# Kernel optimization log

Hardware: AMD Instinct MI355X
Metric: run time of the kernel (lower is better)

## Reference

```python
import jax, jax.numpy as jnp
import numpy as np

# Static graph layout: B equal-size graphs of N nodes; first S nodes of each
# graph are 'sentence' nodes, the remaining N-S are 'other' nodes.
B, N, S, C = 64, 4096, 512, 128
TOTAL = B * N
E = 4_194_304          # avg degree 16
K_SENT = 3             # num_output_sentences
RATIO = 0.5
K_OTHER = int(np.ceil(RATIO * (N - S)))  # 1792 -> 1795 kept nodes per graph


def setup_inputs() -> dict:
    key = jax.random.key(0)
    k1, k2, k3 = jax.random.split(key, 3)
    x = jax.random.normal(k1, (TOTAL, C), dtype=jnp.float32)
    weight = jax.random.uniform(k2, (C,), dtype=jnp.float32)  # torch.rand(1, C)
    edge_index = jax.random.randint(k3, (2, E), 0, TOTAL, dtype=jnp.int32)
    batch = jnp.repeat(jnp.arange(B, dtype=jnp.int32), N)     # per-node graph id
    return {"x": x, "weight": weight, "edge_index": edge_index, "batch": batch}


def _pool(x, weight, edge_index, batch):
    # score_i = tanh(<x_i, w> / ||w||)   (min_score is None branch)
    score = jnp.tanh((x @ weight) / jnp.linalg.norm(weight))        # [TOTAL]
    score_b = score.reshape(B, N)

    # ragged-as-dense per-graph top-k (torch does dense reshape + sort + gather)
    base = (jnp.arange(B, dtype=jnp.int32) * N)[:, None]            # [B,1]
    _, sent_idx = jax.lax.top_k(score_b[:, :S], K_SENT)             # [B,K_SENT]
    _, other_idx = jax.lax.top_k(score_b[:, S:], K_OTHER)           # [B,K_OTHER]
    perm = jnp.concatenate([
        (sent_idx.astype(jnp.int32) + base).reshape(-1),            # all sentence picks first
        (other_idx.astype(jnp.int32) + S + base).reshape(-1),
    ])                                                              # [B*(K_SENT+K_OTHER)]

    x_out = x[perm] * score[perm][:, None]                          # multiplier == 1
    batch_out = batch[perm]

    # filter_adj: remap kept nodes to new ids; drop edges touching dropped nodes.
    node_map = jnp.full((TOTAL,), -1, dtype=jnp.int32).at[perm].set(
        jnp.arange(perm.shape[0], dtype=jnp.int32))
    row = node_map[edge_index[0]]
    col = node_map[edge_index[1]]
    keep = (row >= 0) & (col >= 0)
    # jit-friendly compaction: stable-sort kept edges to the front, pad tail with -1
    order = jnp.argsort(jnp.where(keep, 0, 1), stable=True)
    edge_index_new = jnp.stack([jnp.where(keep, row, -1)[order],
                                jnp.where(keep, col, -1)[order]])
    num_edges = keep.sum()
    return x_out, edge_index_new, batch_out, perm, score[perm], num_edges


def reference(x, weight, edge_index, batch):
    return _pool(x, weight, edge_index, batch)
```

## Files before the change

### kernel.cpp

```cpp
#include <hip/hip_runtime.h>
#include <hip/hip_bf16.h>
#include <stdint.h>

#define NB 64
#define NN 4096
#define NS 512
#define NC 128
#define NTOTAL (NB*NN)
#define NE 4194304
#define KSENT 3
#define KOTHER 1792
#define KPG (KSENT+KOTHER)
#define NP (NB*KPG)
#define NSENT_TOT (NB*KSENT)
#define NOTHER (NN-NS)

#define OFF_X     0ull
#define OFF_EDGE  14704640ull
#define OFF_BATCH 23093248ull
#define OFF_PERM  23208128ull
#define OFF_SCORE 23323008ull
#define OFF_NE    23437888ull

#define NEBLK 512
#define EPB   (NE/NEBLK)
#define STASH 2560

#define NBW   (NTOTAL/32)
#define GBLK  ((NP*NC/4)/256)
#define TBLK  (NE/4/256)

#define FLG_AGG (1ull<<62)
#define FLG_INC (2ull<<62)

__device__ float g_scores[NTOTAL];
__device__ int   g_perm[NP];
__device__ int   g_nodemap[NTOTAL];
__device__ uint32_t g_bits[NBW];
__device__ unsigned long long g_state[NEBLK];
__device__ int   g_total;

__device__ __forceinline__ float bfr(float f){
  uint32_t u = __float_as_uint(f);
  uint32_t r = u + 0x7FFFu + ((u >> 16) & 1u);
  return __uint_as_float(r & 0xFFFF0000u);
}

__device__ __forceinline__ float xla_tanhf(float x){
#pragma clang fp contract(off)
  float xc = fminf(fmaxf(x, -7.90531110763549805f), 7.90531110763549805f);
  float x2 = __fmul_rn(xc, xc);
  float p = -2.76076847742355e-16f;
  p = __fadd_rn(__fmul_rn(p, x2),  2.00018790482477e-13f);
  p = __fadd_rn(__fmul_rn(p, x2), -8.60467152213735e-11f);
  p = __fadd_rn(__fmul_rn(p, x2),  5.12229709037114e-08f);
  p = __fadd_rn(__fmul_rn(p, x2),  1.48572235717979e-05f);
  p = __fadd_rn(__fmul_rn(p, x2),  6.37261928875436e-04f);
  p = __fadd_rn(__fmul_rn(p, x2),  4.89352455891786e-03f);
  p = __fmul_rn(xc, p);
  float q = 1.19825839466702e-06f;
  q = __fadd_rn(__fmul_rn(q, x2), 1.18534705686654e-04f);
  q = __fadd_rn(__fmul_rn(q, x2), 2.26843463243900e-03f);
  q = __fadd_rn(__fmul_rn(q, x2), 4.89352518554385e-03f);
  float r = __fdiv_rn(p, q);
  return (fabsf(x) < 0.0004f) ? x : r;
}

__global__ __launch_bounds__(256) void k_scores(const float* __restrict__ x,
                                                const float* __restrict__ w){
#pragma clang fp contract(off)
  int tid = threadIdx.x;
  int gid = blockIdx.x*256 + tid;
  if (gid < NTOTAL) g_nodemap[gid] = -1;
  if (blockIdx.x == 0){ g_state[tid] = 0ull; g_state[256+tid] = 0ull; }

  int grp = tid >> 4, j = tid & 15;
  int row = blockIdx.x*16 + grp;
  const float* rx = x + (size_t)row*NC;

  float wv[8];
#pragma unroll
  for (int k = 0; k < 8; ++k) wv[k] = w[k*16 + j];

  float an = 0.f, ad = 0.f;
#pragma unroll
  for (int k = 0; k < 8; ++k) an = __fadd_rn(an, __fmul_rn(wv[k], wv[k]));
#pragma unroll
  for (int k = 0; k < 8; ++k) ad = __fadd_rn(ad, __fmul_rn(rx[k*16 + j], wv[k]));

  float o;
  o = __shfl_down(an, 8); if (j < 8) an = __fadd_rn(an, o);
  o = __shfl_down(ad, 8); if (j < 8) ad = __fadd_rn(ad, o);
  o = __shfl_down(an, 4); if (j < 4) an = __fadd_rn(an, o);
  o = __shfl_down(ad, 4); if (j < 4) ad = __fadd_rn(ad, o);
  o = __shfl_down(an, 2); if (j < 2) an = __fadd_rn(an, o);
  o = __shfl_down(ad, 2); if (j < 2) ad = __fadd_rn(ad, o);
  o = __shfl_down(an, 1);
  float o2 = __shfl_down(ad, 1);
  if (j == 0){
    float nrm = __fsqrt_rn(__fadd_rn(an, o));
    float acc = __fadd_rn(ad, o2);
    float t = __fdiv_rn(acc, nrm);
    g_scores[row] = xla_tanhf(t);
  }
}

__device__ __forceinline__ unsigned long long skey(float s, int idx){
  uint32_t u = __float_as_uint(s);
  u = (u & 0x80000000u) ? ~u : (u | 0x80000000u);
  u = ~u;
  return ((unsigned long long)u << 32) | (uint32_t)idx;
}

__global__ __launch_bounds__(512) void k_topk(){
  __shared__ uint32_t keyA[NOTHER], keyB[NOTHER];
  __shared__ uint16_t idxA[NOTHER], idxB[NOTHER], rnk[NOTHER];
  __shared__ uint16_t cnt[8][256];
  __shared__ uint16_t tot[256], dbase[256];
  __shared__ unsigned long long smin[8];
  __shared__ unsigned long long swin;
  __shared__ uint32_t bl[NN/32];

  int g = blockIdx.x, tid = threadIdx.x;
  int lane = tid & 63, wv = tid >> 6;
  const float* sg = g_scores + g*NN;

  if (tid < NN/32) bl[tid] = 0u;
  __syncthreads();

  unsigned long long key = skey(sg[tid], tid);
  for (int t = 0; t < KSENT; ++t){
    unsigned long long v = key;
#pragma unroll
    for (int off = 32; off; off >>= 1){
      unsigned long long o = __shfl_down(v, off);
      v = (o < v) ? o : v;
    }
    if (lane == 0) smin[wv] = v;
    __syncthreads();
    if (tid == 0){
      unsigned long long mm = smin[0];
      for (int w2 = 1; w2 < 8; ++w2) if (smin[w2] < mm) mm = smin[w2];
      swin = mm;
    }
    __syncthreads();
    unsigned long long winner = swin;
    if (key == winner){
      int idx = (int)(winner & 0xFFFFFFFFull);
      int node = g*NN + idx, p = g*KSENT + t;
      g_perm[p] = node;
      g_nodemap[node] = p;
      atomicOr(&bl[idx >> 5], 1u << (idx & 31));
      key = ~0ull;
    }
    __syncthreads();
  }

  for (int i = tid; i < NOTHER; i += 512){
    uint32_t u = __float_as_uint(sg[NS + i]);
    u = (u & 0x80000000u) ? ~u : (u | 0x80000000u);
    keyA[i] = ~u;
    idxA[i] = (uint16_t)i;
  }
  __syncthreads();

  uint32_t* ksrc = keyA; uint32_t* kdst = keyB;
  uint16_t* isrc = idxA; uint16_t* idst = idxB;
  unsigned long long ltmask = (1ull << lane) - 1ull;
  int base = wv * 448;

  for (int pass = 0; pass < 4; ++pass){
    int shift = pass * 8;
    uint32_t* c32 = (uint32_t*)cnt[wv];
    c32[lane] = 0; c32[64 + lane] = 0;
    for (int r = 0; r < 7; ++r){
      int i = base + r*64 + lane;
      uint32_t k = ksrc[i];
      uint32_t d = (k >> shift) & 255u;
      unsigned long long m = ~0ull;
#pragma unroll
      for (int b = 0; b < 8; ++b){
        unsigned long long bb = __ballot((d >> b) & 1u);
        m &= ((d >> b) & 1u) ? bb : ~bb;
      }
      int rir = __popcll(m & ltmask);
      uint16_t bse = cnt[wv][d];
      rnk[i] = (uint16_t)(bse + rir);
      if ((m >> lane) == 1ull)
        cnt[wv][d] = (uint16_t)(bse + __popcll(m));
    }
    __syncthreads();
    if (tid < 256){
      int s = 0;
#pragma unroll
      for (int w2 = 0; w2 < 8; ++w2){
        int t2 = cnt[w2][tid]; cnt[w2][tid] = (uint16_t)s; s += t2;
      }
      tot[tid] = (uint16_t)s;
    }
    __syncthreads();
    if (tid < 64){
      int b4 = tid*4;
      int s0=tot[b4], s1=tot[b4+1], s2=tot[b4+2], s3=tot[b4+3];
      int lsum = s0+s1+s2+s3;
      int sc = lsum;
      for (int off = 1; off < 64; off <<= 1){
        int vv = __shfl_up(sc, off);
        if (lane >= off) sc += vv;
      }
      int excl = sc - lsum;
      dbase[b4]   = (uint16_t)excl;
      dbase[b4+1] = (uint16_t)(excl + s0);
      dbase[b4+2] = (uint16_t)(excl + s0 + s1);
      dbase[b4+3] = (uint16_t)(excl + s0 + s1 + s2);
    }
    __syncthreads();
    {
      int idx = tid;
#pragma unroll
      for (int kk = 0; kk < 4; ++kk){
        int w2 = (idx >> 8) & 7, d2 = idx & 255;
        cnt[w2][d2] = (uint16_t)(cnt[w2][d2] + dbase[d2]);
        idx += 512;
      }
    }
    __syncthreads();
    for (int r = 0; r < 7; ++r){
      int i = base + r*64 + lane;
      uint32_t k = ksrc[i];
      uint32_t d = (k >> shift) & 255u;
      int dest = cnt[wv][d] + rnk[i];
      kdst[dest] = k; idst[dest] = isrc[i];
    }
    __syncthreads();
    uint32_t* tk = ksrc; ksrc = kdst; kdst = tk;
    uint16_t* ti = isrc; isrc = idst; idst = ti;
  }
  for (int j = tid; j < KOTHER; j += 512){
    int li = NS + (int)isrc[j];
    int node = g*NN + li;
    int p = NSENT_TOT + g*KOTHER + j;
    g_perm[p] = node;
    g_nodemap[node] = p;
    atomicOr(&bl[li >> 5], 1u << (li & 31));
  }
  __syncthreads();
  if (tid < NN/32) g_bits[g*(NN/32) + tid] = bl[tid];
}

__global__ __launch_bounds__(256) void k_edges(const int* __restrict__ ei,
                                               float* __restrict__ out){
  __shared__ uint32_t bm[NBW];
  __shared__ int2 rc[STASH];
  __shared__ int wsum[4];
  __shared__ int s_off;
  int b = blockIdx.x, tid = threadIdx.x;
  int lane = tid & 63, wid = tid >> 6;
  int base = b * EPB;
  unsigned long long ltm = (1ull << lane) - 1ull;

  {
    uint4* d4 = (uint4*)bm;
    const uint4* s4 = (const uint4*)g_bits;
#pragma unroll
    for (int kk = 0; kk < 8; ++kk) d4[tid + kk*256] = s4[tid + kk*256];
  }
  if (tid == 0) s_off = 0;
  __syncthreads();

  int running = 0;
  for (int s = 0; s < EPB; s += 256){
    int e = base + s + tid;
    int u = ei[e], v = ei[NE + e];
    bool keep = ((bm[u >> 5] >> (u & 31)) & 1u) &&
                ((bm[v >> 5] >> (v & 31)) & 1u);
    unsigned long long m = __ballot(keep);
    if (lane == 0) wsum[wid] = __popcll(m);
    __syncthreads();
    int wbase = 0;
#pragma unroll
    for (int w2 = 0; w2 < 4; ++w2) if (w2 < wid) wbase += wsum[w2];
    int tot = wsum[0] + wsum[1] + wsum[2] + wsum[3];
    if (keep){
      int lp = running + wbase + __popcll(m & ltm);
      if (lp < STASH){
        int2 p; p.x = g_nodemap[u]; p.y = g_nodemap[v]; rc[lp] = p;
      }
    }
    running += tot;
    __syncthreads();
  }
  int myc = running;

  if (b == 0){
    if (tid == 0)
      atomicExch(&g_state[0], FLG_INC | (unsigned long long)(uint32_t)myc);
  } else if (wid == 0){
    if (lane == 0)
      atomicExch(&g_state[b], FLG_AGG | (unsigned long long)(uint32_t)myc);
    int prev = 0, win = b - 1;
    bool done = false;
    while (!done){
      int idxl = win - lane;
      unsigned long long st = (idxl >= 0) ? atomicAdd(&g_state[idxl], 0ull)
                                          : FLG_INC;
      unsigned f = (unsigned)(st >> 62);
      unsigned long long readym = __ballot(f != 0u);
      unsigned long long incm   = __ballot(f == 2u);
      if (incm){
        int l0 = __ffsll((long long)incm) - 1;
        unsigned long long needm = (l0 == 63) ? ~0ull : ((1ull << (l0+1)) - 1ull);
        if ((readym & needm) == needm){
          int contrib = (lane <= l0) ? (int)(uint32_t)st : 0;
#pragma unroll
          for (int off = 32; off; off >>= 1)
            contrib += __shfl_down(contrib, off);
          if (lane == 0) prev += contrib;
          done = true;
        }
      } else if (readym == ~0ull){
        int contrib = (int)(uint32_t)st;
#pragma unroll
        for (int off = 32; off; off >>= 1)
          contrib += __shfl_down(contrib, off);
        if (lane == 0) prev += contrib;
        win -= 64;
      } else {
        __builtin_amdgcn_s_sleep(2);
      }
    }
    if (lane == 0){
      atomicExch(&g_state[b], FLG_INC | (unsigned long long)(uint32_t)(prev + myc));
      s_off = prev;
      if (b == NEBLK-1){
        g_total = prev + myc;
        out[OFF_NE] = bfr((float)(prev + myc));
      }
    }
  }
  __syncthreads();
  int off = s_off;

  int lim = myc < STASH ? myc : STASH;
  for (int i = tid; i < lim; i += 256){
    int2 p = rc[i];
    out[OFF_EDGE + off + i]      = bfr((float)p.x);
    out[OFF_EDGE + NE + off + i] = bfr((float)p.y);
  }
  if (myc > STASH){
    running = 0;
    __syncthreads();
    for (int s = 0; s < EPB; s += 256){
      int e = base + s + tid;
      int u = ei[e], v = ei[NE + e];
      bool keep = ((bm[u >> 5] >> (u & 31)) & 1u) &&
                  ((bm[v >> 5] >> (v & 31)) & 1u);
      unsigned long long m = __ballot(keep);
      if (lane == 0) wsum[wid] = __popcll(m);
      __syncthreads();
      int wbase = 0;
#pragma unroll
      for (int w2 = 0; w2 < 4; ++w2) if (w2 < wid) wbase += wsum[w2];
      int tot = wsum[0] + wsum[1] + wsum[2] + wsum[3];
      if (keep){
        int lp = running + wbase + __popcll(m & ltm);
        if (lp >= STASH){
          out[OFF_EDGE + off + lp]      = bfr((float)g_nodemap[u]);
          out[OFF_EDGE + NE + off + lp] = bfr((float)g_nodemap[v]);
        }
      }
      running += tot;
      __syncthreads();
    }
  }
}

__global__ __launch_bounds__(256) void k_gather(const float* __restrict__ x,
                                                float* __restrict__ out){
  if (blockIdx.x < GBLK){
    size_t q = (size_t)blockIdx.x*256 + threadIdx.x;
    int p  = (int)(q >> 5);
    int c4 = (int)(q & 31);
    int node = g_perm[p];
    float s = g_scores[node];
    float4 v = *(const float4*)(x + (size_t)node*NC + c4*4);
    float4 o;
    o.x = bfr(__fmul_rn(v.x, s));
    o.y = bfr(__fmul_rn(v.y, s));
    o.z = bfr(__fmul_rn(v.z, s));
    o.w = bfr(__fmul_rn(v.w, s));
    *(float4*)(out + OFF_X + (size_t)p*NC + c4*4) = o;
    if (c4 == 0){
      out[OFF_BATCH + p] = bfr((float)(node >> 12));
      out[OFF_PERM  + p] = bfr((float)node);
      out[OFF_SCORE + p] = bfr(s);
    }
  } else {
    int T = g_total;
    int i4 = (blockIdx.x - GBLK)*256 + threadIdx.x;
    int pos = i4 * 4;
    float4 mv; mv.x = mv.y = mv.z = mv.w = -1.0f;
    if (pos >= T){
      ((float4*)(out + OFF_EDGE))[i4] = mv;
      ((float4*)(out + OFF_EDGE + NE))[i4] = mv;
    } else if (pos + 4 > T){
      for (int k = T; k < pos + 4; ++k){
        out[OFF_EDGE + k] = -1.0f;
        out[OFF_EDGE + NE + k] = -1.0f;
      }
    }
  }
}

extern "C" void kernel_launch(void* const* d_in, const int* in_sizes, int n_in,
                              void* d_out, int out_size, void* d_ws, size_t ws_size,
                              hipStream_t stream) {
  const float* x = (const float*)d_in[0];
  const float* w = (const float*)d_in[1];
  const int*   ei = (const int*)d_in[2];
  float* out = (float*)d_out;

  hipLaunchKernelGGL(k_scores, dim3(NTOTAL/16),    dim3(256), 0, stream, x, w);
  hipLaunchKernelGGL(k_topk,   dim3(NB),           dim3(512), 0, stream);
  hipLaunchKernelGGL(k_edges,  dim3(NEBLK),        dim3(256), 0, stream, ei, out);
  hipLaunchKernelGGL(k_gather, dim3(GBLK + TBLK),  dim3(256), 0, stream, x, out);
}
```

Measured before the change: 108.2 us.

## Fuse four kernels into two with intra-kernel flag waits and overlapped gather

Merges score computation into the top-k kernel. Extra blocks compute scores and signal per-graph completion counters, and top-k blocks spin-wait on those counters. Merges the feature gather into the edge-compaction kernel as extra persistent blocks, and writes the -1 tail padding per block from its own drop count, which removes g_total and the separate pad pass. Edge blocks move to 512 threads. This removes two launches and their serialization boundaries, at the risk of deadlock if the waiting top-k blocks occupy the device before the score blocks are scheduled.

Measured after the change: 230.9 us. 113% more time.

```diff
diff --git a/kernel.cpp b/kernel.cpp
--- a/kernel.cpp
+++ b/kernel.cpp
@@ -25,10 +25,8 @@
 #define NEBLK 512
 #define EPB   (NE/NEBLK)
 #define STASH 2560
-
+#define NGB   1024
 #define NBW   (NTOTAL/32)
-#define GBLK  ((NP*NC/4)/256)
-#define TBLK  (NE/4/256)
 
 #define FLG_AGG (1ull<<62)
 #define FLG_INC (2ull<<62)
@@ -38,7 +36,7 @@
 __device__ int   g_nodemap[NTOTAL];
 __device__ uint32_t g_bits[NBW];
 __device__ unsigned long long g_state[NEBLK];
-__device__ int   g_total;
+__device__ int   g_done[NB];
 
 __device__ __forceinline__ float bfr(float f){
   uint32_t u = __float_as_uint(f);
@@ -66,45 +64,6 @@
   return (fabsf(x) < 0.0004f) ? x : r;
 }
 
-__global__ __launch_bounds__(256) void k_scores(const float* __restrict__ x,
-                                                const float* __restrict__ w){
-#pragma clang fp contract(off)
-  int tid = threadIdx.x;
-  int gid = blockIdx.x*256 + tid;
-  if (gid < NTOTAL) g_nodemap[gid] = -1;
-  if (blockIdx.x == 0){ g_state[tid] = 0ull; g_state[256+tid] = 0ull; }
-
-  int grp = tid >> 4, j = tid & 15;
-  int row = blockIdx.x*16 + grp;
-  const float* rx = x + (size_t)row*NC;
-
-  float wv[8];
-#pragma unroll
-  for (int k = 0; k < 8; ++k) wv[k] = w[k*16 + j];
-
-  float an = 0.f, ad = 0.f;
-#pragma unroll
-  for (int k = 0; k < 8; ++k) an = __fadd_rn(an, __fmul_rn(wv[k], wv[k]));
-#pragma unroll
-  for (int k = 0; k < 8; ++k) ad = __fadd_rn(ad, __fmul_rn(rx[k*16 + j], wv[k]));
-
-  float o;
-  o = __shfl_down(an, 8); if (j < 8) an = __fadd_rn(an, o);
-  o = __shfl_down(ad, 8); if (j < 8) ad = __fadd_rn(ad, o);
-  o = __shfl_down(an, 4); if (j < 4) an = __fadd_rn(an, o);
-  o = __shfl_down(ad, 4); if (j < 4) ad = __fadd_rn(ad, o);
-  o = __shfl_down(an, 2); if (j < 2) an = __fadd_rn(an, o);
-  o = __shfl_down(ad, 2); if (j < 2) ad = __fadd_rn(ad, o);
-  o = __shfl_down(an, 1);
-  float o2 = __shfl_down(ad, 1);
-  if (j == 0){
-    float nrm = __fsqrt_rn(__fadd_rn(an, o));
-    float acc = __fadd_rn(ad, o2);
-    float t = __fdiv_rn(acc, nrm);
-    g_scores[row] = xla_tanhf(t);
-  }
-}
-
 __device__ __forceinline__ unsigned long long skey(float s, int idx){
   uint32_t u = __float_as_uint(s);
   u = (u & 0x80000000u) ? ~u : (u | 0x80000000u);
@@ -112,7 +71,8 @@
   return ((unsigned long long)u << 32) | (uint32_t)idx;
 }
 
-__global__ __launch_bounds__(512) void k_topk(){
+__global__ __launch_bounds__(512, 4) void k1(const float* __restrict__ x,
+                                             const float* __restrict__ w){
   __shared__ uint32_t keyA[NOTHER], keyB[NOTHER];
   __shared__ uint16_t idxA[NOTHER], idxB[NOTHER], rnk[NOTHER];
   __shared__ uint16_t cnt[8][256];
@@ -121,8 +81,66 @@
   __shared__ unsigned long long swin;
   __shared__ uint32_t bl[NN/32];
 
-  int g = blockIdx.x, tid = threadIdx.x;
+  int b = blockIdx.x, tid = threadIdx.x;
   int lane = tid & 63, wv = tid >> 6;
+
+  if (b >= NB){
+#pragma clang fp contract(off)
+    int pb = b - NB;
+    g_state[pb] = 0ull;
+    int row0 = pb * 512;
+    g_nodemap[row0 + tid] = -1;
+
+    int grp = tid >> 4, j = tid & 15;
+    float wvv[8];
+#pragma unroll
+    for (int k = 0; k < 8; ++k) wvv[k] = w[k*16 + j];
+
+    float an = 0.f;
+#pragma unroll
+    for (int k = 0; k < 8; ++k) an = __fadd_rn(an, __fmul_rn(wvv[k], wvv[k]));
+    float o;
+    o = __shfl_down(an, 8); if (j < 8) an = __fadd_rn(an, o);
+    o = __shfl_down(an, 4); if (j < 4) an = __fadd_rn(an, o);
+    o = __shfl_down(an, 2); if (j < 2) an = __fadd_rn(an, o);
+    o = __shfl_down(an, 1);
+    float nrm = __fsqrt_rn(__fadd_rn(an, o));
+
+    for (int it = 0; it < 16; ++it){
+      int row = row0 + it*32 + grp;
+      const float* rx = x + (size_t)row*NC;
+      float ad = 0.f;
+#pragma unroll
+      for (int k = 0; k < 8; ++k)
+        ad = __fadd_rn(ad, __fmul_rn(rx[k*16 + j], wvv[k]));
+      o = __shfl_down(ad, 8); if (j < 8) ad = __fadd_rn(ad, o);
+      o = __shfl_down(ad, 4); if (j < 4) ad = __fadd_rn(ad, o);
+      o = __shfl_down(ad, 2); if (j < 2) ad = __fadd_rn(ad, o);
+      o = __shfl_down(ad, 1);
+      if (j == 0){
+        float t = __fdiv_rn(__fadd_rn(ad, o), nrm);
+        g_scores[row] = xla_tanhf(t);
+      }
+    }
+    __threadfence();
+    __syncthreads();
+    if (tid == 0)
+      __hip_atomic_fetch_add(&g_done[pb >> 3], 1, __ATOMIC_RELEASE,
+                             __HIP_MEMORY_SCOPE_AGENT);
+    return;
+  }
+
+  int g = b;
+  if (tid == 0){
+    while (__hip_atomic_load(&g_done[g], __ATOMIC_ACQUIRE,
+                             __HIP_MEMORY_SCOPE_AGENT) < 8)
+      __builtin_amdgcn_s_sleep(4);
+    __hip_atomic_store(&g_done[g], 0, __ATOMIC_RELAXED,
+                       __HIP_MEMORY_SCOPE_AGENT);
+  }
+  __syncthreads();
+  __threadfence();
+
   const float* sg = g_scores + g*NN;
 
   if (tid < NN/32) bl[tid] = 0u;
@@ -133,8 +151,8 @@
     unsigned long long v = key;
 #pragma unroll
     for (int off = 32; off; off >>= 1){
-      unsigned long long o = __shfl_down(v, off);
-      v = (o < v) ? o : v;
+      unsigned long long o2 = __shfl_down(v, off);
+      v = (o2 < v) ? o2 : v;
     }
     if (lane == 0) smin[wv] = v;
     __syncthreads();
@@ -179,9 +197,9 @@
       uint32_t d = (k >> shift) & 255u;
       unsigned long long m = ~0ull;
 #pragma unroll
-      for (int b = 0; b < 8; ++b){
-        unsigned long long bb = __ballot((d >> b) & 1u);
-        m &= ((d >> b) & 1u) ? bb : ~bb;
+      for (int bb = 0; bb < 8; ++bb){
+        unsigned long long bm2 = __ballot((d >> bb) & 1u);
+        m &= ((d >> bb) & 1u) ? bm2 : ~bm2;
       }
       int rir = __popcll(m & ltmask);
       uint16_t bse = cnt[wv][d];
@@ -236,10 +254,10 @@
     uint32_t* tk = ksrc; ksrc = kdst; kdst = tk;
     uint16_t* ti = isrc; isrc = idst; idst = ti;
   }
-  for (int j = tid; j < KOTHER; j += 512){
-    int li = NS + (int)isrc[j];
+  for (int jj = tid; jj < KOTHER; jj += 512){
+    int li = NS + (int)isrc[jj];
     int node = g*NN + li;
-    int p = NSENT_TOT + g*KOTHER + j;
+    int p = NSENT_TOT + g*KOTHER + jj;
     g_perm[p] = node;
     g_nodemap[node] = p;
     atomicOr(&bl[li >> 5], 1u << (li & 31));
@@ -248,13 +266,39 @@
   if (tid < NN/32) g_bits[g*(NN/32) + tid] = bl[tid];
 }
 
-__global__ __launch_bounds__(256) void k_edges(const int* __restrict__ ei,
-                                               float* __restrict__ out){
+__global__ __launch_bounds__(512, 6) void k2(const int* __restrict__ ei,
+                                             const float* __restrict__ x,
+                                             float* __restrict__ out){
   __shared__ uint32_t bm[NBW];
   __shared__ int2 rc[STASH];
-  __shared__ int wsum[4];
+  __shared__ int wsum[8];
   __shared__ int s_off;
   int b = blockIdx.x, tid = threadIdx.x;
+
+  if (b >= NEBLK){
+    const size_t total4 = (size_t)NP*NC/4;
+    for (size_t q = (size_t)(b - NEBLK)*512 + tid; q < total4;
+         q += (size_t)NGB*512){
+      int p  = (int)(q >> 5);
+      int c4 = (int)(q & 31);
+      int node = g_perm[p];
+      float s = g_scores[node];
+      float4 v = *(const float4*)(x + (size_t)node*NC + c4*4);
+      float4 o;
+      o.x = bfr(__fmul_rn(v.x, s));
+      o.y = bfr(__fmul_rn(v.y, s));
+      o.z = bfr(__fmul_rn(v.z, s));
+      o.w = bfr(__fmul_rn(v.w, s));
+      *(float4*)(out + OFF_X + (size_t)p*NC + c4*4) = o;
+      if (c4 == 0){
+        out[OFF_BATCH + p] = bfr((float)(node >> 12));
+        out[OFF_PERM  + p] = bfr((float)node);
+        out[OFF_SCORE + p] = bfr(s);
+      }
+    }
+    return;
+  }
+
   int lane = tid & 63, wid = tid >> 6;
   int base = b * EPB;
   unsigned long long ltm = (1ull << lane) - 1ull;
@@ -263,13 +307,13 @@
     uint4* d4 = (uint4*)bm;
     const uint4* s4 = (const uint4*)g_bits;
 #pragma unroll
-    for (int kk = 0; kk < 8; ++kk) d4[tid + kk*256] = s4[tid + kk*256];
+    for (int kk = 0; kk < 4; ++kk) d4[tid + kk*512] = s4[tid + kk*512];
   }
   if (tid == 0) s_off = 0;
   __syncthreads();
 
   int running = 0;
-  for (int s = 0; s < EPB; s += 256){
+  for (int s = 0; s < EPB; s += 512){
     int e = base + s + tid;
     int u = ei[e], v = ei[NE + e];
     bool keep = ((bm[u >> 5] >> (u & 31)) & 1u) &&
@@ -279,8 +323,10 @@
     __syncthreads();
     int wbase = 0;
 #pragma unroll
-    for (int w2 = 0; w2 < 4; ++w2) if (w2 < wid) wbase += wsum[w2];
-    int tot = wsum[0] + wsum[1] + wsum[2] + wsum[3];
+    for (int w2 = 0; w2 < 8; ++w2) if (w2 < wid) wbase += wsum[w2];
+    int tot = 0;
+#pragma unroll
+    for (int w2 = 0; w2 < 8; ++w2) tot += wsum[w2];
     if (keep){
       int lp = running + wbase + __popcll(m & ltm);
       if (lp < STASH){
@@ -332,17 +378,15 @@
     if (lane == 0){
       atomicExch(&g_state[b], FLG_INC | (unsigned long long)(uint32_t)(prev + myc));
       s_off = prev;
-      if (b == NEBLK-1){
-        g_total = prev + myc;
+      if (b == NEBLK-1)
         out[OFF_NE] = bfr((float)(prev + myc));
-      }
     }
   }
   __syncthreads();
   int off = s_off;
 
   int lim = myc < STASH ? myc : STASH;
-  for (int i = tid; i < lim; i += 256){
+  for (int i = tid; i < lim; i += 512){
     int2 p = rc[i];
     out[OFF_EDGE + off + i]      = bfr((float)p.x);
     out[OFF_EDGE + NE + off + i] = bfr((float)p.y);
@@ -350,7 +394,7 @@
   if (myc > STASH){
     running = 0;
     __syncthreads();
-    for (int s = 0; s < EPB; s += 256){
+    for (int s = 0; s < EPB; s += 512){
       int e = base + s + tid;
       int u = ei[e], v = ei[NE + e];
       bool keep = ((bm[u >> 5] >> (u & 31)) & 1u) &&
@@ -360,8 +404,10 @@
       __syncthreads();
       int wbase = 0;
 #pragma unroll
-      for (int w2 = 0; w2 < 4; ++w2) if (w2 < wid) wbase += wsum[w2];
-      int tot = wsum[0] + wsum[1] + wsum[2] + wsum[3];
+      for (int w2 = 0; w2 < 8; ++w2) if (w2 < wid) wbase += wsum[w2];
+      int tot = 0;
+#pragma unroll
+      for (int w2 = 0; w2 < 8; ++w2) tot += wsum[w2];
       if (keep){
         int lp = running + wbase + __popcll(m & ltm);
         if (lp >= STASH){
@@ -373,42 +419,13 @@
       __syncthreads();
     }
   }
-}
-
-__global__ __launch_bounds__(256) void k_gather(const float* __restrict__ x,
-                                                float* __restrict__ out){
-  if (blockIdx.x < GBLK){
-    size_t q = (size_t)blockIdx.x*256 + threadIdx.x;
-    int p  = (int)(q >> 5);
-    int c4 = (int)(q & 31);
-    int node = g_perm[p];
-    float s = g_scores[node];
-    float4 v = *(const float4*)(x + (size_t)node*NC + c4*4);
-    float4 o;
-    o.x = bfr(__fmul_rn(v.x, s));
-    o.y = bfr(__fmul_rn(v.y, s));
-    o.z = bfr(__fmul_rn(v.z, s));
-    o.w = bfr(__fmul_rn(v.w, s));
-    *(float4*)(out + OFF_X + (size_t)p*NC + c4*4) = o;
-    if (c4 == 0){
-      out[OFF_BATCH + p] = bfr((float)(node >> 12));
-      out[OFF_PERM  + p] = bfr((float)node);
-      out[OFF_SCORE + p] = bfr(s);
-    }
-  } else {
-    int T = g_total;
-    int i4 = (blockIdx.x - GBLK)*256 + threadIdx.x;
-    int pos = i4 * 4;
-    float4 mv; mv.x = mv.y = mv.z = mv.w = -1.0f;
-    if (pos >= T){
-      ((float4*)(out + OFF_EDGE))[i4] = mv;
-      ((float4*)(out + OFF_EDGE + NE))[i4] = mv;
-    } else if (pos + 4 > T){
-      for (int k = T; k < pos + 4; ++k){
-        out[OFF_EDGE + k] = -1.0f;
-        out[OFF_EDGE + NE + k] = -1.0f;
-      }
-    }
+
+  int drops = EPB - myc;
+  int dropoff = base - off;
+  int t0 = NE - dropoff - drops;
+  for (int i = tid; i < drops; i += 512){
+    out[OFF_EDGE + t0 + i]      = -1.0f;
+    out[OFF_EDGE + NE + t0 + i] = -1.0f;
   }
 }
 
@@ -420,8 +437,6 @@
   const int*   ei = (const int*)d_in[2];
   float* out = (float*)d_out;
 
-  hipLaunchKernelGGL(k_scores, dim3(NTOTAL/16),    dim3(256), 0, stream, x, w);
-  hipLaunchKernelGGL(k_topk,   dim3(NB),           dim3(512), 0, stream);
-  hipLaunchKernelGGL(k_edges,  dim3(NEBLK),        dim3(256), 0, stream, ei, out);
-  hipLaunchKernelGGL(k_gather, dim3(GBLK + TBLK),  dim3(256), 0, stream, x, out);
-}
+  hipLaunchKernelGGL(k1, dim3(NB + 512),     dim3(512), 0, stream, x, w);
+  hipLaunchKernelGGL(k2, dim3(NEBLK + NGB),  dim3(512), 0, stream, ei, x, out);
+}
```

## Fuse edge compaction, feature gather and tail fill into one kernel

Applied to the files above, without the earlier changes.

Merges the edge-filter kernel and the gather kernel into a single launch. The first 512 blocks compact edges and the remaining 1024 blocks grid-stride over the feature gather. Each edge block now writes its own segment of -1 padding using its exclusive offset, so the global edge total no longer has to be read by a later kernel. Edge blocks move to 512 threads. This removes one launch and the serialization between compaction and gather, at the cost of the two workloads sharing CUs and the decoupled-lookback scan possibly waiting on blocks that are delayed behind gather blocks.

Result: faster. 90.98 us (median of 2 runs) (-15.9%).

```diff
diff --git a/kernel.cpp b/kernel.cpp
--- a/kernel.cpp
+++ b/kernel.cpp
@@ -25,10 +25,8 @@
 #define NEBLK 512
 #define EPB   (NE/NEBLK)
 #define STASH 2560
-
+#define NGB   1024
 #define NBW   (NTOTAL/32)
-#define GBLK  ((NP*NC/4)/256)
-#define TBLK  (NE/4/256)
 
 #define FLG_AGG (1ull<<62)
 #define FLG_INC (2ull<<62)
@@ -38,7 +36,6 @@
 __device__ int   g_nodemap[NTOTAL];
 __device__ uint32_t g_bits[NBW];
 __device__ unsigned long long g_state[NEBLK];
-__device__ int   g_total;
 
 __device__ __forceinline__ float bfr(float f){
   uint32_t u = __float_as_uint(f);
@@ -248,13 +245,39 @@
   if (tid < NN/32) g_bits[g*(NN/32) + tid] = bl[tid];
 }
 
-__global__ __launch_bounds__(256) void k_edges(const int* __restrict__ ei,
-                                               float* __restrict__ out){
+__global__ __launch_bounds__(512) void k2(const int* __restrict__ ei,
+                                          const float* __restrict__ x,
+                                          float* __restrict__ out){
   __shared__ uint32_t bm[NBW];
   __shared__ int2 rc[STASH];
-  __shared__ int wsum[4];
+  __shared__ int wsum[8];
   __shared__ int s_off;
   int b = blockIdx.x, tid = threadIdx.x;
+
+  if (b >= NEBLK){
+    const size_t total4 = (size_t)NP*NC/4;
+    for (size_t q = (size_t)(b - NEBLK)*512 + tid; q < total4;
+         q += (size_t)NGB*512){
+      int p  = (int)(q >> 5);
+      int c4 = (int)(q & 31);
+      int node = g_perm[p];
+      float s = g_scores[node];
+      float4 v = *(const float4*)(x + (size_t)node*NC + c4*4);
+      float4 o;
+      o.x = bfr(__fmul_rn(v.x, s));
+      o.y = bfr(__fmul_rn(v.y, s));
+      o.z = bfr(__fmul_rn(v.z, s));
+      o.w = bfr(__fmul_rn(v.w, s));
+      *(float4*)(out + OFF_X + (size_t)p*NC + c4*4) = o;
+      if (c4 == 0){
+        out[OFF_BATCH + p] = bfr((float)(node >> 12));
+        out[OFF_PERM  + p] = bfr((float)node);
+        out[OFF_SCORE + p] = bfr(s);
+      }
+    }
+    return;
+  }
+
   int lane = tid & 63, wid = tid >> 6;
   int base = b * EPB;
   unsigned long long ltm = (1ull << lane) - 1ull;
@@ -263,13 +286,13 @@
     uint4* d4 = (uint4*)bm;
     const uint4* s4 = (const uint4*)g_bits;
 #pragma unroll
-    for (int kk = 0; kk < 8; ++kk) d4[tid + kk*256] = s4[tid + kk*256];
+    for (int kk = 0; kk < 4; ++kk) d4[tid + kk*512] = s4[tid + kk*512];
   }
   if (tid == 0) s_off = 0;
   __syncthreads();
 
   int running = 0;
-  for (int s = 0; s < EPB; s += 256){
+  for (int s = 0; s < EPB; s += 512){
     int e = base + s + tid;
     int u = ei[e], v = ei[NE + e];
     bool keep = ((bm[u >> 5] >> (u & 31)) & 1u) &&
@@ -279,8 +302,10 @@
     __syncthreads();
     int wbase = 0;
 #pragma unroll
-    for (int w2 = 0; w2 < 4; ++w2) if (w2 < wid) wbase += wsum[w2];
-    int tot = wsum[0] + wsum[1] + wsum[2] + wsum[3];
+    for (int w2 = 0; w2 < 8; ++w2) if (w2 < wid) wbase += wsum[w2];
+    int tot = 0;
+#pragma unroll
+    for (int w2 = 0; w2 < 8; ++w2) tot += wsum[w2];
     if (keep){
       int lp = running + wbase + __popcll(m & ltm);
       if (lp < STASH){
@@ -332,17 +357,15 @@
     if (lane == 0){
       atomicExch(&g_state[b], FLG_INC | (unsigned long long)(uint32_t)(prev + myc));
       s_off = prev;
-      if (b == NEBLK-1){
-        g_total = prev + myc;
+      if (b == NEBLK-1)
         out[OFF_NE] = bfr((float)(prev + myc));
-      }
     }
   }
   __syncthreads();
   int off = s_off;
 
   int lim = myc < STASH ? myc : STASH;
-  for (int i = tid; i < lim; i += 256){
+  for (int i = tid; i < lim; i += 512){
     int2 p = rc[i];
     out[OFF_EDGE + off + i]      = bfr((float)p.x);
     out[OFF_EDGE + NE + off + i] = bfr((float)p.y);
@@ -350,7 +373,7 @@
   if (myc > STASH){
     running = 0;
     __syncthreads();
-    for (int s = 0; s < EPB; s += 256){
+    for (int s = 0; s < EPB; s += 512){
       int e = base + s + tid;
       int u = ei[e], v = ei[NE + e];
       bool keep = ((bm[u >> 5] >> (u & 31)) & 1u) &&
@@ -360,8 +383,10 @@
       __syncthreads();
       int wbase = 0;
 #pragma unroll
-      for (int w2 = 0; w2 < 4; ++w2) if (w2 < wid) wbase += wsum[w2];
-      int tot = wsum[0] + wsum[1] + wsum[2] + wsum[3];
+      for (int w2 = 0; w2 < 8; ++w2) if (w2 < wid) wbase += wsum[w2];
+      int tot = 0;
+#pragma unroll
+      for (int w2 = 0; w2 < 8; ++w2) tot += wsum[w2];
       if (keep){
         int lp = running + wbase + __popcll(m & ltm);
         if (lp >= STASH){
@@ -373,42 +398,13 @@
       __syncthreads();
     }
   }
-}
-
-__global__ __launch_bounds__(256) void k_gather(const float* __restrict__ x,
-                                                float* __restrict__ out){
-  if (blockIdx.x < GBLK){
-    size_t q = (size_t)blockIdx.x*256 + threadIdx.x;
-    int p  = (int)(q >> 5);
-    int c4 = (int)(q & 31);
-    int node = g_perm[p];
-    float s = g_scores[node];
-    float4 v = *(const float4*)(x + (size_t)node*NC + c4*4);
-    float4 o;
-    o.x = bfr(__fmul_rn(v.x, s));
-    o.y = bfr(__fmul_rn(v.y, s));
-    o.z = bfr(__fmul_rn(v.z, s));
-    o.w = bfr(__fmul_rn(v.w, s));
-    *(float4*)(out + OFF_X + (size_t)p*NC + c4*4) = o;
-    if (c4 == 0){
-      out[OFF_BATCH + p] = bfr((float)(node >> 12));
-      out[OFF_PERM  + p] = bfr((float)node);
-      out[OFF_SCORE + p] = bfr(s);
-    }
-  } else {
-    int T = g_total;
-    int i4 = (blockIdx.x - GBLK)*256 + threadIdx.x;
-    int pos = i4 * 4;
-    float4 mv; mv.x = mv.y = mv.z = mv.w = -1.0f;
-    if (pos >= T){
-      ((float4*)(out + OFF_EDGE))[i4] = mv;
-      ((float4*)(out + OFF_EDGE + NE))[i4] = mv;
-    } else if (pos + 4 > T){
-      for (int k = T; k < pos + 4; ++k){
-        out[OFF_EDGE + k] = -1.0f;
-        out[OFF_EDGE + NE + k] = -1.0f;
-      }
-    }
+
+  int drops = EPB - myc;
+  int dropoff = base - off;
+  int t0 = NE - dropoff - drops;
+  for (int i = tid; i < drops; i += 512){
+    out[OFF_EDGE + t0 + i]      = -1.0f;
+    out[OFF_EDGE + NE + t0 + i] = -1.0f;
   }
 }
 
@@ -420,8 +416,7 @@
   const int*   ei = (const int*)d_in[2];
   float* out = (float*)d_out;
 
-  hipLaunchKernelGGL(k_scores, dim3(NTOTAL/16),    dim3(256), 0, stream, x, w);
-  hipLaunchKernelGGL(k_topk,   dim3(NB),           dim3(512), 0, stream);
-  hipLaunchKernelGGL(k_edges,  dim3(NEBLK),        dim3(256), 0, stream, ei, out);
-  hipLaunchKernelGGL(k_gather, dim3(GBLK + TBLK),  dim3(256), 0, stream, x, out);
-}
+  hipLaunchKernelGGL(k_scores, dim3(NTOTAL/16),   dim3(256), 0, stream, x, w);
+  hipLaunchKernelGGL(k_topk,   dim3(NB),          dim3(512), 0, stream);
+  hipLaunchKernelGGL(k2,       dim3(NEBLK + NGB), dim3(512), 0, stream, ei, x, out);
+}
```
